# Kernel optimization log

Measured on AMD Instinct MI355X. Metric: run time of the kernel, lower is better.

The kernel has to match this reference:

```python
import math
import jax, jax.numpy as jnp
import numpy as np

D_MODEL = 1024
NUM_HEADS = 16
D_HEAD = D_MODEL // NUM_HEADS  # 64
K_S = 32  # sparse top-k keys kept per query
B, N = 2, 2048


def setup_inputs() -> dict:
    key = jax.random.key(0)
    ks = jax.random.split(key, 9)
    s = 1.0 / math.sqrt(D_MODEL)
    return {
        "x": jax.random.normal(ks[0], (B, N, D_MODEL), dtype=jnp.float32),
        "Wq": jax.random.normal(ks[1], (D_MODEL, D_MODEL), dtype=jnp.float32) * s,
        "bq": jnp.zeros((D_MODEL,), dtype=jnp.float32),
        "Wk": jax.random.normal(ks[2], (D_MODEL, D_MODEL), dtype=jnp.float32) * s,
        "bk": jnp.zeros((D_MODEL,), dtype=jnp.float32),
        "Wv": jax.random.normal(ks[3], (D_MODEL, D_MODEL), dtype=jnp.float32) * s,
        "bv": jnp.zeros((D_MODEL,), dtype=jnp.float32),
        "Wo": jax.random.normal(ks[4], (D_MODEL, D_MODEL), dtype=jnp.float32) * s,
        "bo": jnp.zeros((D_MODEL,), dtype=jnp.float32),
    }


def _attn(x, Wq, bq, Wk, bk, Wv, bv, Wo, bo):
    b, n, _ = x.shape
    # projections (torch Linear: y = x W^T + b)
    q = (x @ Wq.T + bq).reshape(b, n, NUM_HEADS, D_HEAD).transpose(0, 2, 1, 3)
    k = (x @ Wk.T + bk).reshape(b, n, NUM_HEADS, D_HEAD).transpose(0, 2, 1, 3)
    v = (x @ Wv.T + bv).reshape(b, n, NUM_HEADS, D_HEAD).transpose(0, 2, 1, 3)
    # full scores [b, H, n, n]
    scores = jnp.einsum("bhqd,bhkd->bhqk", q, k) / math.sqrt(D_HEAD)
    # causal mask (triu above diagonal -> -inf)
    causal = jnp.triu(jnp.ones((n, n), dtype=bool), k=1)
    neg_inf = jnp.array(-jnp.inf, dtype=scores.dtype)
    scores = jnp.where(causal, neg_inf, scores)
    # sparse top-k: keep only K_S largest scores per query row
    vals, idx = jax.lax.top_k(scores, K_S)
    masked = jnp.full_like(scores, -jnp.inf)
    masked = jnp.put_along_axis(masked, idx, vals, axis=-1, inplace=False)
    attn = jax.nn.softmax(masked, axis=-1)  # dropout p=0.0 -> identity
    out = jnp.einsum("bhqk,bhkd->bhqd", attn, v)
    out = out.transpose(0, 2, 1, 3).reshape(b, n, D_MODEL)
    y = out @ Wo.T + bo
    return y, attn.mean(axis=1)


def reference(x, Wq, bq, Wk, bk, Wv, bv, Wo, bo):
    return _attn(x, Wq, bq, Wk, bk, Wv, bv, Wo, bo)
```

## Files before the change

kernel.cpp:

```cpp
#include <hip/hip_runtime.h>
#include <hip/hip_bf16.h>
#include <math.h>

#define BATCH   2
#define NTOK    2048
#define DMODEL  1024
#define HEADS   16
#define DHEAD   64
#define KSEL    32
#define MROWS   (BATCH * NTOK)
#define NBLK8   (NTOK / 8)
#define TPW     8

typedef short     bf16x8 __attribute__((ext_vector_type(8)));
typedef float     f32x4  __attribute__((ext_vector_type(4)));
typedef unsigned short ushort_t;
typedef unsigned long long u64;

#define GLOAD_LDS16(g, l) \
    __builtin_amdgcn_global_load_lds((const __attribute__((address_space(1))) void*)(g), \
                                     (__attribute__((address_space(3))) void*)(l), 16, 0, 0)

__device__ __forceinline__ ushort_t f2bf(float f) {
    unsigned u = __float_as_uint(f);
    unsigned r = (u + 0x7FFFu + ((u >> 16) & 1u)) >> 16;
    return (ushort_t)r;
}
__device__ __forceinline__ float bf2f(ushort_t h) {
    return __uint_as_float(((unsigned)h) << 16);
}

__global__ __launch_bounds__(256) void conv_split(const float* __restrict__ in,
                                                  ushort_t* __restrict__ hi,
                                                  ushort_t* __restrict__ lo, int n)
{
    const int i = (blockIdx.x * 256 + threadIdx.x) * 4;
    if (i + 3 < n) {
        const float4 v = *(const float4*)(in + i);
        ushort4 ph, pl;
        ph.x = f2bf(v.x); pl.x = f2bf(v.x - bf2f(ph.x));
        ph.y = f2bf(v.y); pl.y = f2bf(v.y - bf2f(ph.y));
        ph.z = f2bf(v.z); pl.z = f2bf(v.z - bf2f(ph.z));
        ph.w = f2bf(v.w); pl.w = f2bf(v.w - bf2f(ph.w));
        *(ushort4*)(hi + i) = ph;
        *(ushort4*)(lo + i) = pl;
    }
}

__global__ __launch_bounds__(256) void zero_fill(float* __restrict__ p, int n4)
{
    const int i = blockIdx.x * 256 + threadIdx.x;
    if (i < n4) ((float4*)p)[i] = (float4){0.f, 0.f, 0.f, 0.f};
}

__device__ __forceinline__ unsigned mono_key(float f) {
    const unsigned u = __float_as_uint(f);
    return (u ^ (unsigned)(((int)u >> 31) | 0x80000000)) + 1u;
}
__device__ __forceinline__ float unmono(unsigned m) {
    const unsigned u = m - 1u;
    return __uint_as_float(u ^ (unsigned)(((int)(~u) >> 31) | 0x80000000));
}

__global__ __launch_bounds__(256) void gemm_split_mfma(const ushort_t* __restrict__ Ahi,
                                                       const ushort_t* __restrict__ Alo,
                                                       const ushort_t* __restrict__ Bhi,
                                                       const ushort_t* __restrict__ Blo,
                                                       const float* __restrict__ bias,
                                                       float* __restrict__ out,
                                                       ushort_t* __restrict__ oh,
                                                       ushort_t* __restrict__ om,
                                                       ushort_t* __restrict__ ol,
                                                       int mode)
{
    __shared__ ushort_t AbufH[128 * 32];
    __shared__ ushort_t AbufL[128 * 32];
    __shared__ ushort_t BbufH[64 * 32];
    __shared__ ushort_t BbufL[64 * 32];

    const int tid  = threadIdx.x;
    const int wave = tid >> 6;
    const int lane = tid & 63;
    const int m0 = blockIdx.x * 128;
    const int n0 = blockIdx.y * 64;

    f32x4 acc[2][4];
#pragma unroll
    for (int i = 0; i < 2; ++i)
#pragma unroll
        for (int j = 0; j < 4; ++j) acc[i][j] = (f32x4){0.f, 0.f, 0.f, 0.f};

    const int ar0 = tid >> 2;
    const int ar1 = 64 + (tid >> 2);
    const int ak  = (tid & 3) << 3;
    const int br  = tid >> 2;

    const int fr = lane & 15;
    const int fk = (lane >> 4) << 3;

    for (int k0 = 0; k0 < DMODEL; k0 += 32) {
        __syncthreads();
        const size_t aoff0 = (size_t)(m0 + ar0) * DMODEL + k0 + ak;
        const size_t aoff1 = (size_t)(m0 + ar1) * DMODEL + k0 + ak;
        const size_t boff  = (size_t)(n0 + br) * DMODEL + k0 + ak;
        GLOAD_LDS16(Ahi + aoff0, AbufH + (size_t)tid * 8);
        GLOAD_LDS16(Ahi + aoff1, AbufH + (size_t)(256 + tid) * 8);
        GLOAD_LDS16(Alo + aoff0, AbufL + (size_t)tid * 8);
        GLOAD_LDS16(Alo + aoff1, AbufL + (size_t)(256 + tid) * 8);
        GLOAD_LDS16(Bhi + boff, BbufH + (size_t)tid * 8);
        GLOAD_LDS16(Blo + boff, BbufL + (size_t)tid * 8);
        __syncthreads();

        bf16x8 afh[2], afl[2], bfh[4], bfl[4];
#pragma unroll
        for (int mi = 0; mi < 2; ++mi) {
            const int ro = (wave * 32 + mi * 16 + fr) * 32 + fk;
            afh[mi] = *(const bf16x8*)(AbufH + ro);
            afl[mi] = *(const bf16x8*)(AbufL + ro);
        }
#pragma unroll
        for (int ni = 0; ni < 4; ++ni) {
            const int ro = (ni * 16 + fr) * 32 + fk;
            bfh[ni] = *(const bf16x8*)(BbufH + ro);
            bfl[ni] = *(const bf16x8*)(BbufL + ro);
        }

#pragma unroll
        for (int mi = 0; mi < 2; ++mi)
#pragma unroll
            for (int ni = 0; ni < 4; ++ni) {
                acc[mi][ni] = __builtin_amdgcn_mfma_f32_16x16x32_bf16(afh[mi], bfl[ni], acc[mi][ni], 0, 0, 0);
                acc[mi][ni] = __builtin_amdgcn_mfma_f32_16x16x32_bf16(afl[mi], bfh[ni], acc[mi][ni], 0, 0, 0);
                acc[mi][ni] = __builtin_amdgcn_mfma_f32_16x16x32_bf16(afh[mi], bfh[ni], acc[mi][ni], 0, 0, 0);
            }
    }

#pragma unroll
    for (int ni = 0; ni < 4; ++ni) {
        const int o = n0 + ni * 16 + (lane & 15);
        const float bv = bias[o];
#pragma unroll
        for (int mi = 0; mi < 2; ++mi) {
#pragma unroll
            for (int reg = 0; reg < 4; ++reg) {
                const int m = m0 + wave * 32 + mi * 16 + ((lane >> 4) << 2) + reg;
                const float v = acc[mi][ni][reg] + bv;
                if (mode == 0) {
                    out[(size_t)m * DMODEL + o] = v;
                } else {
                    const int bb = m >> 11;
                    const int n  = m & 2047;
                    const int hd = o >> 6;
                    const int d  = o & 63;
                    const size_t off = (((size_t)(bb * HEADS + hd)) * NTOK + n) * DHEAD + d;
                    if (mode == 1) {
                        out[off] = v;
                    } else {
                        const ushort_t h1 = f2bf(v);
                        const float r1 = v - bf2f(h1);
                        const ushort_t m1 = f2bf(r1);
                        const ushort_t l1 = f2bf(r1 - bf2f(m1));
                        oh[off] = h1; om[off] = m1; ol[off] = l1;
                    }
                }
            }
        }
    }
}

__global__ __launch_bounds__(256, 3) void score_mfma(const ushort_t* __restrict__ Qh,
                                                     const ushort_t* __restrict__ Qm,
                                                     const ushort_t* __restrict__ Ql,
                                                     const ushort_t* __restrict__ Kh,
                                                     const ushort_t* __restrict__ Km,
                                                     const ushort_t* __restrict__ Kl,
                                                     unsigned* __restrict__ S,
                                                     unsigned* __restrict__ Smax,
                                                     int q0, int QC)
{
    const int ks = blockIdx.x;
    const int qt = blockIdx.y;
    const int bh = blockIdx.z;
    const int qbase = q0 + qt * 128;
    const int ktmax = ((qbase + 127) >> 6) + 1;
    const int kt0 = ks * TPW;
    if (kt0 >= ktmax) return;
    const int kt1 = (kt0 + TPW < ktmax) ? (kt0 + TPW) : ktmax;

    __shared__ ushort_t smem[24576];

    const int tid  = threadIdx.x;
    const int wave = tid >> 6;
    const int lane = tid & 63;
    const int l15  = lane & 15;
    const int l4   = lane >> 4;

    const size_t qgbase = ((size_t)bh * NTOK + qbase) * DHEAD;

    {
        const ushort_t* Qp0 = Qh; const ushort_t* Qp1 = Qm; const ushort_t* Qp2 = Ql;
#pragma unroll
        for (int i = 0; i < 4; ++i) {
            const int c = i * 256 + tid;
            const int row = c >> 3;
            const int g = (c & 7) ^ (row & 7);
            const size_t goff = qgbase + (size_t)row * DHEAD + g * 8;
            GLOAD_LDS16(Qp0 + goff, smem + 0 * 8192 + (size_t)c * 8);
            GLOAD_LDS16(Qp1 + goff, smem + 1 * 8192 + (size_t)c * 8);
            GLOAD_LDS16(Qp2 + goff, smem + 2 * 8192 + (size_t)c * 8);
        }
    }
    __syncthreads();

    bf16x8 qf[3][2][2];
#pragma unroll
    for (int p = 0; p < 3; ++p)
#pragma unroll
        for (int j = 0; j < 2; ++j) {
            const int r = wave * 32 + j * 16 + l15;
#pragma unroll
            for (int h = 0; h < 2; ++h) {
                const int slot = (h * 4 + l4) ^ (r & 7);
                qf[p][j][h] = *(const bf16x8*)(smem + p * 8192 + (size_t)(r * 8 + slot) * 8);
            }
        }
    __syncthreads();

#define STAGE_K(bufsel, ktv) do {                                              \
        const size_t kg_ = ((size_t)bh * NTOK + (ktv) * 64) * DHEAD;           \
        _Pragma("unroll")                                                      \
        for (int i_ = 0; i_ < 2; ++i_) {                                       \
            const int c_ = i_ * 256 + tid;                                     \
            const int row_ = c_ >> 3;                                          \
            const int g_ = (c_ & 7) ^ (row_ & 7);                              \
            const size_t goff_ = kg_ + (size_t)row_ * DHEAD + g_ * 8;          \
            ushort_t* dst_ = smem + (bufsel) * 12288 + (size_t)c_ * 8;         \
            GLOAD_LDS16(Kh + goff_, dst_ + 0 * 4096);                          \
            GLOAD_LDS16(Km + goff_, dst_ + 1 * 4096);                          \
            GLOAD_LDS16(Kl + goff_, dst_ + 2 * 4096);                          \
        }                                                                      \
    } while (0)

    STAGE_K(0, kt0);
    int cur = 0;

    const size_t srowQ = (size_t)bh * QC;

    for (int kt = kt0; kt < kt1; ++kt) {
        __syncthreads();
        if (kt + 1 < kt1) STAGE_K(cur ^ 1, kt + 1);

        f32x4 acc[4][2];
#pragma unroll
        for (int m = 0; m < 4; ++m)
#pragma unroll
            for (int j = 0; j < 2; ++j) acc[m][j] = (f32x4){0.f, 0.f, 0.f, 0.f};

        const ushort_t* kb = smem + cur * 12288;
#pragma unroll
        for (int h = 0; h < 2; ++h) {
            bf16x8 kf[4];
#pragma unroll
            for (int m = 0; m < 4; ++m) {
                const int r = m * 16 + l15;
                const int slot = (h * 4 + l4) ^ (r & 7);
                kf[m] = *(const bf16x8*)(kb + 0 * 4096 + (size_t)(r * 8 + slot) * 8);
            }
#pragma unroll
            for (int m = 0; m < 4; ++m)
#pragma unroll
                for (int j = 0; j < 2; ++j) {
                    acc[m][j] = __builtin_amdgcn_mfma_f32_16x16x32_bf16(kf[m], qf[2][j][h], acc[m][j], 0, 0, 0);
                    acc[m][j] = __builtin_amdgcn_mfma_f32_16x16x32_bf16(kf[m], qf[1][j][h], acc[m][j], 0, 0, 0);
                    acc[m][j] = __builtin_amdgcn_mfma_f32_16x16x32_bf16(kf[m], qf[0][j][h], acc[m][j], 0, 0, 0);
                }
#pragma unroll
            for (int m = 0; m < 4; ++m) {
                const int r = m * 16 + l15;
                const int slot = (h * 4 + l4) ^ (r & 7);
                kf[m] = *(const bf16x8*)(kb + 1 * 4096 + (size_t)(r * 8 + slot) * 8);
            }
#pragma unroll
            for (int m = 0; m < 4; ++m)
#pragma unroll
                for (int j = 0; j < 2; ++j) {
                    acc[m][j] = __builtin_amdgcn_mfma_f32_16x16x32_bf16(kf[m], qf[1][j][h], acc[m][j], 0, 0, 0);
                    acc[m][j] = __builtin_amdgcn_mfma_f32_16x16x32_bf16(kf[m], qf[0][j][h], acc[m][j], 0, 0, 0);
                }
#pragma unroll
            for (int m = 0; m < 4; ++m) {
                const int r = m * 16 + l15;
                const int slot = (h * 4 + l4) ^ (r & 7);
                kf[m] = *(const bf16x8*)(kb + 2 * 4096 + (size_t)(r * 8 + slot) * 8);
            }
#pragma unroll
            for (int m = 0; m < 4; ++m)
#pragma unroll
                for (int j = 0; j < 2; ++j)
                    acc[m][j] = __builtin_amdgcn_mfma_f32_16x16x32_bf16(kf[m], qf[0][j][h], acc[m][j], 0, 0, 0);
        }

#pragma unroll
        for (int j = 0; j < 2; ++j) {
            const int qrow  = wave * 32 + j * 16 + l15;
            const int qlrow = qt * 128 + qrow;
            const int qglob = qbase + qrow;
            const size_t srow = (srowQ + qlrow) * NTOK;
            const size_t mrow = (srowQ + qlrow) * NBLK8;
#pragma unroll
            for (int m = 0; m < 4; ++m) {
                const int kcol0 = kt * 64 + m * 16 + (l4 << 2);
                uint4 kv;
                kv.x = mono_key(acc[m][j][0] * 0.125f);
                kv.y = mono_key(acc[m][j][1] * 0.125f);
                kv.z = mono_key(acc[m][j][2] * 0.125f);
                kv.w = mono_key(acc[m][j][3] * 0.125f);
                *(uint4*)(S + srow + kcol0) = kv;
                unsigned cm = (kcol0     <= qglob) ? kv.x : 0u;
                unsigned t;
                t = (kcol0 + 1 <= qglob) ? kv.y : 0u; cm = (t > cm) ? t : cm;
                t = (kcol0 + 2 <= qglob) ? kv.z : 0u; cm = (t > cm) ? t : cm;
                t = (kcol0 + 3 <= qglob) ? kv.w : 0u; cm = (t > cm) ? t : cm;
                const unsigned o = __shfl_xor(cm, 16, 64);
                cm = (o > cm) ? o : cm;
                if ((lane & 16) == 0) {
                    const int gblk = kt * 8 + m * 2 + (lane >> 5);
                    Smax[mrow + gblk] = cm;
                }
            }
        }
        cur ^= 1;
    }
#undef STAGE_K
}

__global__ __launch_bounds__(256) void select_v6(const unsigned* __restrict__ S,
                                                 const unsigned* __restrict__ Smax,
                                                 const float* __restrict__ V,
                                                 float* __restrict__ ctx,
                                                 float* __restrict__ attn,
                                                 int q0, int QC)
{
    __shared__ int   sBlkAll[4][KSEL];
    __shared__ int   sIdxAll[4][KSEL];
    __shared__ float sEAll[4][KSEL];

    const int lane = threadIdx.x & 63;
    const int wave = threadIdx.x >> 6;
    const int ql = blockIdx.x;
    const int b  = blockIdx.y >> 2;
    const int hg = blockIdx.y & 3;
    const int h  = hg * 4 + wave;
    const int q  = q0 + ql;
    const int L  = q + 1;
    const int nsel = (L < KSEL) ? L : KSEL;
    const int nb = (L + 7) >> 3;

    const size_t bhx = (size_t)(b * HEADS + h);
    const unsigned* Srow = S + (bhx * QC + ql) * NTOK;
    const unsigned* Mrow = Smax + (bhx * QC + ql) * NBLK8;
    const float* Vb   = V + bhx * NTOK * DHEAD;
    float* ctxRow  = ctx + (((size_t)(b * NTOK + q)) * HEADS + h) * DHEAD;
    float* attnRow = attn + ((size_t)(b * NTOK + q)) * NTOK;
    int*   sBlk = sBlkAll[wave];
    int*   sIdx = sIdxAll[wave];
    float* sE   = sEAll[wave];

    const uint4 bm4 = *(const uint4*)(Mrow + lane * 4);
    unsigned bmax[4] = {bm4.x, bm4.y, bm4.z, bm4.w};
#pragma unroll
    for (int s = 0; s < 4; ++s)
        if (lane * 4 + s >= nb) bmax[s] = 0u;

    unsigned gmax = bmax[0];
    gmax = (bmax[1] > gmax) ? bmax[1] : gmax;
    gmax = (bmax[2] > gmax) ? bmax[2] : gmax;
    gmax = (bmax[3] > gmax) ? bmax[3] : gmax;
#pragma unroll
    for (int d = 1; d < 64; d <<= 1) {
        const unsigned o = __shfl_xor(gmax, d, 64);
        gmax = (o > gmax) ? o : gmax;
    }
    const float vmax = unmono(gmax);

    unsigned selb = 0u;
    unsigned blkLo = 1u;
    int nselb;
    if (nb <= KSEL) {
        nselb = nb;
#pragma unroll
        for (int s = 0; s < 4; ++s)
            if (lane * 4 + s < nb) selb |= 1u << s;
    } else {
        nselb = KSEL;
        unsigned lo = 1u, hi = gmax >> 16;
        while (lo < hi) {
            const unsigned mid = lo + ((hi - lo + 1u) >> 1);
            const unsigned midk = mid << 16;
            int cnt = 0;
#pragma unroll
            for (int s = 0; s < 4; ++s)
                cnt += __popcll(__ballot(bmax[s] >= midk));
            if (cnt >= KSEL) lo = mid; else hi = mid - 1u;
        }
        blkLo = lo;
        const unsigned Tkb = lo << 16;
        const unsigned Gkb = Tkb | 0xFFFFu;
        int cge = 0, cgt = 0;
#pragma unroll
        for (int s = 0; s < 4; ++s) {
            cge += __popcll(__ballot(bmax[s] >= Tkb));
            cgt += __popcll(__ballot(bmax[s] > Gkb));
        }
        if (cge == KSEL) {
#pragma unroll
            for (int s = 0; s < 4; ++s)
                selb |= (bmax[s] >= Tkb) ? (1u << s) : 0u;
        } else {
            unsigned bmb = 0u;
#pragma unroll
            for (int s = 0; s < 4; ++s) {
                selb |= (bmax[s] > Gkb) ? (1u << s) : 0u;
                bmb  |= (bmax[s] >= Tkb && bmax[s] <= Gkb) ? (1u << s) : 0u;
            }
            int k_tie = KSEL - cgt;
            while (k_tie > 0) {
                u64 best = 0;
                unsigned bmm = bmb;
                while (bmm) {
                    const int s = __builtin_ctz(bmm);
                    bmm &= bmm - 1u;
                    const unsigned gblk = (unsigned)(lane * 4 + s);
                    const u64 k = ((u64)bmax[s] << 32) | (unsigned)~gblk;
                    if (k > best) best = k;
                }
                u64 bb = best;
#pragma unroll
                for (int d = 1; d < 64; d <<= 1) {
                    const u64 o = __shfl_xor(bb, d, 64);
                    bb = (o > bb) ? o : bb;
                }
                const unsigned gblk = ~(unsigned)bb;
                if (lane == (int)(gblk >> 2)) {
                    const unsigned bit = 1u << (gblk & 3u);
                    selb |= bit;
                    bmb &= ~bit;
                }
                --k_tie;
            }
        }
    }

    {
        const int cb = __popc(selb);
        int pfxb = cb;
#pragma unroll
        for (int d = 1; d < 64; d <<= 1) {
            const int t = __shfl_up(pfxb, d, 64);
            if (lane >= d) pfxb += t;
        }
        pfxb -= cb;
        unsigned mskb = selb;
        int posb = pfxb;
        while (mskb) {
            const int s = __builtin_ctz(mskb);
            mskb &= mskb - 1u;
            sBlk[posb++] = lane * 4 + s;
        }
    }
    __asm volatile("s_waitcnt lgkmcnt(0)" ::: "memory");

    const int NC = nselb * 8;
    unsigned km[4];
    int idx[4];
#pragma unroll
    for (int c = 0; c < 4; ++c) {
        const int t = c * 64 + lane;
        unsigned m = 0u;
        int j = 0;
        if (t < NC) {
            const int blk = sBlk[t >> 3];
            j = blk * 8 + (t & 7);
            if (j < L) m = Srow[j];
        }
        km[c] = m;
        idx[c] = j;
    }

    unsigned lo = blkLo, hi = gmax >> 16;
    while (lo < hi) {
        const unsigned mid = lo + ((hi - lo + 1u) >> 1);
        const unsigned midk = mid << 16;
        int cnt = 0;
#pragma unroll
        for (int c = 0; c < 4; ++c)
            cnt += __popcll(__ballot(km[c] >= midk));
        if (cnt >= nsel) lo = mid; else hi = mid - 1u;
    }
    const unsigned Tk = lo << 16;
    const unsigned Gk = Tk | 0xFFFFu;

    int cnt_ge = 0, cnt_gt = 0;
#pragma unroll
    for (int c = 0; c < 4; ++c) {
        cnt_ge += __popcll(__ballot(km[c] >= Tk));
        cnt_gt += __popcll(__ballot(km[c] > Gk));
    }

    unsigned selmask = 0u;
    if (cnt_ge == nsel) {
#pragma unroll
        for (int c = 0; c < 4; ++c)
            selmask |= (km[c] >= Tk) ? (1u << c) : 0u;
    } else {
        unsigned bmask = 0u;
#pragma unroll
        for (int c = 0; c < 4; ++c) {
            selmask |= (km[c] > Gk) ? (1u << c) : 0u;
            bmask   |= (km[c] >= Tk && km[c] <= Gk) ? (1u << c) : 0u;
        }
        int k_tie = nsel - cnt_gt;
        while (k_tie > 0) {
            u64 best = 0;
            unsigned bmm = bmask;
            while (bmm) {
                const int c = __builtin_ctz(bmm);
                bmm &= bmm - 1u;
                const int t = c * 64 + lane;
                const u64 k = ((u64)km[c] << 32) |
                              ((u64)(0xFFFFu ^ (unsigned)idx[c]) << 16) | (u64)t;
                if (k > best) best = k;
            }
            u64 bb = best;
#pragma unroll
            for (int d = 1; d < 64; d <<= 1) {
                const u64 o = __shfl_xor(bb, d, 64);
                bb = (o > bb) ? o : bb;
            }
            const unsigned tt = (unsigned)bb & 0xFFFFu;
            if (lane == (int)(tt & 63u)) {
                const unsigned bit = 1u << (tt >> 6);
                selmask |= bit;
                bmask &= ~bit;
            }
            --k_tie;
        }
    }

    const int csel = __popc(selmask);
    int pfx = csel;
#pragma unroll
    for (int d = 1; d < 64; d <<= 1) {
        const int t = __shfl_up(pfx, d, 64);
        if (lane >= d) pfx += t;
    }
    pfx -= csel;

    float esum = 0.f;
    unsigned msk = selmask;
    int pos = pfx;
    while (msk) {
        const int c = __builtin_ctz(msk);
        msk &= msk - 1u;
        const float e = __expf(unmono(km[c]) - vmax);
        esum += e;
        sIdx[pos] = idx[c];
        sE[pos] = e;
        ++pos;
    }

    float Z = esum;
#pragma unroll
    for (int d = 1; d < 64; d <<= 1) Z += __shfl_xor(Z, d, 64);
    const float rcpZ = 1.0f / Z;

    msk = selmask;
    pos = pfx;
    while (msk) {
        const int c = __builtin_ctz(msk);
        msk &= msk - 1u;
        const float w = sE[pos] * rcpZ;
        ++pos;
        atomicAdd(&attnRow[idx[c]], w * (1.0f / (float)HEADS));
    }

    float acc = 0.f;
    for (int i = 0; i < nsel; ++i) {
        const int id = sIdx[i];
        const float wi = sE[i] * rcpZ;
        acc += wi * Vb[(size_t)id * DHEAD + lane];
    }
    ctxRow[lane] = acc;
}

extern "C" void kernel_launch(void* const* d_in, const int* in_sizes, int n_in,
                              void* d_out, int out_size, void* d_ws, size_t ws_size,
                              hipStream_t stream) {
    const float* x  = (const float*)d_in[0];
    const float* Wq = (const float*)d_in[1];
    const float* bq = (const float*)d_in[2];
    const float* Wk = (const float*)d_in[3];
    const float* bk = (const float*)d_in[4];
    const float* Wv = (const float*)d_in[5];
    const float* bv = (const float*)d_in[6];
    const float* Wo = (const float*)d_in[7];
    const float* bo = (const float*)d_in[8];

    const size_t MB = 1ull << 20;
    char* wsb = (char*)d_ws;
    float*    Vws = (float*)(wsb + 0 * MB);
    float*    ctx = (float*)(wsb + 16 * MB);
    ushort_t* xhi = (ushort_t*)(wsb + 32 * MB);
    ushort_t* xlo = (ushort_t*)(wsb + 40 * MB);
    ushort_t* wqh = (ushort_t*)(wsb + 48 * MB);
    ushort_t* wql = (ushort_t*)(wsb + 50 * MB);
    ushort_t* wkh = (ushort_t*)(wsb + 52 * MB);
    ushort_t* wkl = (ushort_t*)(wsb + 54 * MB);
    ushort_t* wvh = (ushort_t*)(wsb + 56 * MB);
    ushort_t* wvl = (ushort_t*)(wsb + 58 * MB);
    ushort_t* woh = (ushort_t*)(wsb + 60 * MB);
    ushort_t* wol = (ushort_t*)(wsb + 62 * MB);
    ushort_t* Qh  = (ushort_t*)(wsb + 64 * MB);
    ushort_t* Qm  = (ushort_t*)(wsb + 72 * MB);
    ushort_t* Ql  = (ushort_t*)(wsb + 80 * MB);
    ushort_t* Kh  = (ushort_t*)(wsb + 88 * MB);
    ushort_t* Km  = (ushort_t*)(wsb + 96 * MB);
    ushort_t* Kl  = (ushort_t*)(wsb + 104 * MB);
    ushort_t* cxh = xhi;
    ushort_t* cxl = xlo;

    float* y    = (float*)d_out;
    float* attn = y + (size_t)BATCH * NTOK * DMODEL;

    const int NX = MROWS * DMODEL;
    const int NW = DMODEL * DMODEL;

    conv_split<<<NX / (256 * 4), 256, 0, stream>>>(x, xhi, xlo, NX);
    conv_split<<<NW / (256 * 4), 256, 0, stream>>>(Wq, wqh, wql, NW);
    conv_split<<<NW / (256 * 4), 256, 0, stream>>>(Wk, wkh, wkl, NW);
    conv_split<<<NW / (256 * 4), 256, 0, stream>>>(Wv, wvh, wvl, NW);
    conv_split<<<NW / (256 * 4), 256, 0, stream>>>(Wo, woh, wol, NW);

    dim3 ggrid(MROWS / 128, DMODEL / 64);
    gemm_split_mfma<<<ggrid, 256, 0, stream>>>(xhi, xlo, wqh, wql, bq, nullptr, Qh, Qm, Ql, 2);
    gemm_split_mfma<<<ggrid, 256, 0, stream>>>(xhi, xlo, wkh, wkl, bk, nullptr, Kh, Km, Kl, 2);
    gemm_split_mfma<<<ggrid, 256, 0, stream>>>(xhi, xlo, wvh, wvl, bv, Vws, nullptr, nullptr, nullptr, 1);

    const size_t base_bytes = 112 * MB;
    const size_t avail = (ws_size > base_bytes) ? ws_size - base_bytes : 0;
    int QC = 128;
    for (int cand = NTOK; cand >= 128; cand >>= 1) {
        const size_t need = (size_t)BATCH * HEADS * cand * (size_t)(NTOK + NBLK8) * sizeof(unsigned);
        if (need <= avail) { QC = cand; break; }
    }
    unsigned* Smax = (unsigned*)(wsb + base_bytes);
    unsigned* Sws  = (unsigned*)(wsb + base_bytes +
                                 (size_t)BATCH * HEADS * QC * NBLK8 * sizeof(unsigned));

    const int nattn4 = BATCH * NTOK * NTOK / 4;
    zero_fill<<<(nattn4 + 255) / 256, 256, 0, stream>>>(attn, nattn4);
    for (int q0 = 0; q0 < NTOK; q0 += QC) {
        const int ktm = (q0 + QC) >> 6;
        dim3 sgrid((ktm + TPW - 1) / TPW, QC / 128, BATCH * HEADS);
        score_mfma<<<sgrid, 256, 0, stream>>>(Qh, Qm, Ql, Kh, Km, Kl, Sws, Smax, q0, QC);
        dim3 selgrid(QC, BATCH * 4);
        select_v6<<<selgrid, 256, 0, stream>>>(Sws, Smax, Vws, ctx, attn, q0, QC);
    }

    conv_split<<<NX / (256 * 4), 256, 0, stream>>>(ctx, cxh, cxl, NX);
    gemm_split_mfma<<<ggrid, 256, 0, stream>>>(cxh, cxl, woh, wol, bo, y, nullptr, nullptr, nullptr, 0);
}
```

Before: 553.5 us.

## Double-buffer split-bf16 GEMM LDS tiles with XOR swizzle and occupancy hint

The split-precision MFMA GEMM now uses two LDS stages. The next k-tile is loaded asynchronously with global_load_lds while MFMAs run on the current tile, which cuts the loop from two barriers per k-step to one. The 16-byte chunks in each LDS row are XOR-swizzled by row index to reduce bank conflicts on the fragment reads. launch_bounds asks for two blocks per CU. The cost is double the LDS footprint, which may limit occupancy, and extra register pressure.

```diff
diff --git a/kernel.cpp b/kernel.cpp
--- a/kernel.cpp
+++ b/kernel.cpp
@@ -62,25 +62,24 @@
     return __uint_as_float(u ^ (unsigned)(((int)(~u) >> 31) | 0x80000000));
 }
 
-__global__ __launch_bounds__(256) void gemm_split_mfma(const ushort_t* __restrict__ Ahi,
-                                                       const ushort_t* __restrict__ Alo,
-                                                       const ushort_t* __restrict__ Bhi,
-                                                       const ushort_t* __restrict__ Blo,
-                                                       const float* __restrict__ bias,
-                                                       float* __restrict__ out,
-                                                       ushort_t* __restrict__ oh,
-                                                       ushort_t* __restrict__ om,
-                                                       ushort_t* __restrict__ ol,
-                                                       int mode)
+__global__ __launch_bounds__(256, 2) void gemm_split_mfma(const ushort_t* __restrict__ Ahi,
+                                                          const ushort_t* __restrict__ Alo,
+                                                          const ushort_t* __restrict__ Bhi,
+                                                          const ushort_t* __restrict__ Blo,
+                                                          const float* __restrict__ bias,
+                                                          float* __restrict__ out,
+                                                          ushort_t* __restrict__ oh,
+                                                          ushort_t* __restrict__ om,
+                                                          ushort_t* __restrict__ ol,
+                                                          int mode)
 {
-    __shared__ ushort_t AbufH[128 * 32];
-    __shared__ ushort_t AbufL[128 * 32];
-    __shared__ ushort_t BbufH[64 * 32];
-    __shared__ ushort_t BbufL[64 * 32];
+    __shared__ ushort_t smem[2 * 12288];
 
     const int tid  = threadIdx.x;
     const int wave = tid >> 6;
     const int lane = tid & 63;
+    const int fr   = lane & 15;
+    const int k8   = lane >> 4;
     const int m0 = blockIdx.x * 128;
     const int n0 = blockIdx.y * 64;
 
@@ -90,39 +89,49 @@
 #pragma unroll
         for (int j = 0; j < 4; ++j) acc[i][j] = (f32x4){0.f, 0.f, 0.f, 0.f};
 
-    const int ar0 = tid >> 2;
-    const int ar1 = 64 + (tid >> 2);
-    const int ak  = (tid & 3) << 3;
-    const int br  = tid >> 2;
-
-    const int fr = lane & 15;
-    const int fk = (lane >> 4) << 3;
+#define STAGE(bufsel, k0v) do {                                                \
+        ushort_t* dst_ = smem + (bufsel) * 12288;                              \
+        _Pragma("unroll")                                                      \
+        for (int i_ = 0; i_ < 2; ++i_) {                                       \
+            const int c_ = i_ * 256 + tid;                                     \
+            const int row_ = c_ >> 2;                                          \
+            const int g_ = (c_ & 3) ^ ((row_ >> 1) & 3);                       \
+            const size_t ga_ = (size_t)(m0 + row_) * DMODEL + (k0v) + g_ * 8;  \
+            GLOAD_LDS16(Ahi + ga_, dst_ + (size_t)c_ * 8);                     \
+            GLOAD_LDS16(Alo + ga_, dst_ + 4096 + (size_t)c_ * 8);              \
+        }                                                                      \
+        {                                                                      \
+            const int c_ = tid;                                                \
+            const int row_ = c_ >> 2;                                          \
+            const int g_ = (c_ & 3) ^ ((row_ >> 1) & 3);                       \
+            const size_t gb_ = (size_t)(n0 + row_) * DMODEL + (k0v) + g_ * 8;  \
+            GLOAD_LDS16(Bhi + gb_, dst_ + 8192 + (size_t)c_ * 8);              \
+            GLOAD_LDS16(Blo + gb_, dst_ + 10240 + (size_t)c_ * 8);             \
+        }                                                                      \
+    } while (0)
+
+    STAGE(0, 0);
+    int cur = 0;
 
     for (int k0 = 0; k0 < DMODEL; k0 += 32) {
         __syncthreads();
-        const size_t aoff0 = (size_t)(m0 + ar0) * DMODEL + k0 + ak;
-        const size_t aoff1 = (size_t)(m0 + ar1) * DMODEL + k0 + ak;
-        const size_t boff  = (size_t)(n0 + br) * DMODEL + k0 + ak;
-        GLOAD_LDS16(Ahi + aoff0, AbufH + (size_t)tid * 8);
-        GLOAD_LDS16(Ahi + aoff1, AbufH + (size_t)(256 + tid) * 8);
-        GLOAD_LDS16(Alo + aoff0, AbufL + (size_t)tid * 8);
-        GLOAD_LDS16(Alo + aoff1, AbufL + (size_t)(256 + tid) * 8);
-        GLOAD_LDS16(Bhi + boff, BbufH + (size_t)tid * 8);
-        GLOAD_LDS16(Blo + boff, BbufL + (size_t)tid * 8);
-        __syncthreads();
-
+        if (k0 + 32 < DMODEL) STAGE(cur ^ 1, k0 + 32);
+
+        const ushort_t* buf = smem + cur * 12288;
         bf16x8 afh[2], afl[2], bfh[4], bfl[4];
 #pragma unroll
         for (int mi = 0; mi < 2; ++mi) {
-            const int ro = (wave * 32 + mi * 16 + fr) * 32 + fk;
-            afh[mi] = *(const bf16x8*)(AbufH + ro);
-            afl[mi] = *(const bf16x8*)(AbufL + ro);
+            const int r = wave * 32 + mi * 16 + fr;
+            const int ro = r * 32 + (k8 ^ ((r >> 1) & 3)) * 8;
+            afh[mi] = *(const bf16x8*)(buf + ro);
+            afl[mi] = *(const bf16x8*)(buf + 4096 + ro);
         }
 #pragma unroll
         for (int ni = 0; ni < 4; ++ni) {
-            const int ro = (ni * 16 + fr) * 32 + fk;
-            bfh[ni] = *(const bf16x8*)(BbufH + ro);
-            bfl[ni] = *(const bf16x8*)(BbufL + ro);
+            const int r = ni * 16 + fr;
+            const int ro = r * 32 + (k8 ^ ((r >> 1) & 3)) * 8;
+            bfh[ni] = *(const bf16x8*)(buf + 8192 + ro);
+            bfl[ni] = *(const bf16x8*)(buf + 10240 + ro);
         }
 
 #pragma unroll
@@ -133,7 +142,9 @@
                 acc[mi][ni] = __builtin_amdgcn_mfma_f32_16x16x32_bf16(afl[mi], bfh[ni], acc[mi][ni], 0, 0, 0);
                 acc[mi][ni] = __builtin_amdgcn_mfma_f32_16x16x32_bf16(afh[mi], bfh[ni], acc[mi][ni], 0, 0, 0);
             }
-    }
+        cur ^= 1;
+    }
+#undef STAGE
 
 #pragma unroll
     for (int ni = 0; ni < 4; ++ni) {
```

Measured after the change: 549.5 us. Within noise of the previous version (-0.7%).
